# Performance work log

Hardware: AMD Instinct MI355X
Metric: run time of the kernel (lower is better)

The kernel has to match this reference:

```python
import jax, jax.numpy as jnp
import numpy as np

N_HEADS = 8
D_MODEL = 256
HEAD_DEPTH = D_MODEL // N_HEADS
B, S = 2, 4096


def setup_inputs() -> dict:
    key = jax.random.key(0)
    ks = jax.random.split(key, 8)
    scale = 1.0 / np.sqrt(D_MODEL)
    return {
        "q": jax.random.normal(ks[0], (B, S, D_MODEL), dtype=jnp.float32),
        "k": jax.random.normal(ks[1], (B, S, D_MODEL), dtype=jnp.float32),
        "v": jax.random.normal(ks[2], (B, S, D_MODEL), dtype=jnp.float32),
        "mask": jax.random.randint(ks[3], (B, S, S), 0, 2).astype(jnp.bool_),
        "wq": jax.random.normal(ks[4], (D_MODEL, D_MODEL), dtype=jnp.float32) * scale,
        "wk": jax.random.normal(ks[5], (D_MODEL, D_MODEL), dtype=jnp.float32) * scale,
        "wv": jax.random.normal(ks[6], (D_MODEL, D_MODEL), dtype=jnp.float32) * scale,
        "w_out": jax.random.normal(ks[7], (D_MODEL, D_MODEL), dtype=jnp.float32) * scale,
    }


def _split_heads(x):
    # [B, S, D] -> [B, H, S, Dh]
    b, s, _ = x.shape
    return x.reshape(b, s, N_HEADS, HEAD_DEPTH).transpose(0, 2, 1, 3)


def reference(q, k, v, mask, wq, wk, wv, w_out):
    Q = _split_heads(q @ wq)
    K = _split_heads(k @ wk)
    V = _split_heads(v @ wv)
    # [B, H, Sq, Sk]
    scores = jnp.einsum('bhqd,bhkd->bhqk', Q, K) / jnp.sqrt(
        jnp.asarray(HEAD_DEPTH, dtype=Q.dtype))
    # mask True -> -inf, broadcast over heads
    scores = jnp.where(mask[:, None, :, :], -jnp.inf, scores)
    probs = jax.nn.softmax(scores, axis=-1)
    attn = jnp.einsum('bhqk,bhkd->bhqd', probs, V)
    attn = attn.transpose(0, 2, 1, 3).reshape(q.shape[0], -1, D_MODEL)
    return attn @ w_out
```

## Files before the change

kernel.cpp:

```cpp
#include <hip/hip_runtime.h>
#include <stdint.h>

typedef __bf16 bf16;
typedef __bf16 bf16x8 __attribute__((ext_vector_type(8)));
typedef __bf16 bf16x4 __attribute__((ext_vector_type(4)));
typedef float  f32x4  __attribute__((ext_vector_type(4)));
typedef float  f32x8  __attribute__((ext_vector_type(8)));
typedef float  f32x16 __attribute__((ext_vector_type(16)));
typedef float  float4v __attribute__((ext_vector_type(4)));
typedef int    int4v   __attribute__((ext_vector_type(4)));
typedef unsigned int uint;
typedef unsigned long long ull;

#define QSCALE 0.25505003984214403f


__global__ __launch_bounds__(256) void transpose_w(
    const float* __restrict__ w0, const float* __restrict__ w1,
    const float* __restrict__ w2, const float* __restrict__ w3,
    bf16* __restrict__ WT) {
  const int wsel = blockIdx.z;
  const float* W = wsel == 0 ? w0 : wsel == 1 ? w1 : wsel == 2 ? w2 : w3;
  const int k0 = blockIdx.x * 64, n0 = blockIdx.y * 64;
  __shared__ __align__(16) bf16 t[64][72];
  const int tid = threadIdx.x;
  {
    const int kk = (tid >> 4) << 2;
    const int nn = (tid & 15) << 2;
#pragma unroll
    for (int r = 0; r < 4; ++r) {
      float4v a = *(const float4v*)(W + (size_t)(k0 + kk + r) * 256 + n0 + nn);
#pragma unroll
      for (int j = 0; j < 4; ++j) t[nn + j][kk + r] = (bf16)a[j];
    }
  }
  __syncthreads();
  {
    const int ni = tid >> 2;
    const int c  = (tid & 3) * 16;
    bf16x8 o0 = *(const bf16x8*)(&t[ni][c]);
    bf16x8 o1 = *(const bf16x8*)(&t[ni][c + 8]);
    bf16* dst = WT + (size_t)wsel * 65536 + (size_t)(n0 + ni) * 256 + k0 + c;
    *(bf16x8*)dst = o0;
    *(bf16x8*)(dst + 8) = o1;
  }
}

__global__ __launch_bounds__(256) void proj_pack(
    const float* __restrict__ xq, const float* __restrict__ xk, const float* __restrict__ xv,
    const bf16* __restrict__ WT,
    bf16* __restrict__ Qp, bf16* __restrict__ Kp, bf16* __restrict__ Vp,
    const int* __restrict__ mask, uint* __restrict__ M2) {
  __shared__ __align__(16) unsigned char smem[18432];
  const int tid = threadIdx.x;

  if (blockIdx.x >= 768) {
    uint* lds32 = (uint*)smem;
    const int pid = blockIdx.x - 768;
    const int bb = pid >> 8;
    const int qt = (pid >> 2) & 63, kc = pid & 3;
    const int q0 = qt * 64;
    const int w = tid >> 6, l = tid & 63;
#pragma unroll 2
    for (int r = 0; r < 16; ++r) {
      const int row = w * 16 + r;
      const size_t rowbase = ((size_t)(bb * 4096 + q0 + row)) * 4096 + kc * 1024;
      uint u = 0;
#pragma unroll
      for (int i = 0; i < 4; ++i) {
        int4v m = *(const int4v*)(mask + rowbase + i * 256 + l * 4);
        uint nib = (m[0] != 0 ? 1u : 0u) | (m[1] != 0 ? 2u : 0u) |
                   (m[2] != 0 ? 4u : 0u) | (m[3] != 0 ? 8u : 0u);
        u |= nib << (i * 8);
      }
      lds32[row * 65 + l] = u;
    }
    __syncthreads();
    {
      const int q = tid & 63, kg = tid >> 6;
      const uint* lrow = lds32 + q * 65;
      const int sh = kg * 8;
      uint* o = M2 + ((size_t)(bb * 128 + kc * 32 + kg * 8)) * 4096 + q0 + q;
#pragma unroll
      for (int j = 0; j < 8; ++j) {
        uint d = 0;
#pragma unroll
        for (int jj = 0; jj < 8; ++jj) {
          const uint wv = lrow[j * 8 + jj];
          d |= ((wv >> sh) & 0xFu) << (jj * 4);
        }
        o[(size_t)j * 4096] = d;
      }
    }
    return;
  }

  const int z = blockIdx.x >> 8;
  const int r8 = blockIdx.x & 255;
  const int m0 = (r8 >> 1) * 64, n0 = (r8 & 1) * 128;
  const float* X = z == 0 ? xq : (z == 1 ? xk : xv);
  const bf16* wt = WT + (size_t)z * 65536;
  const int wave = tid >> 6, lane = tid & 63;
  const int nl = lane & 15, quad = lane >> 4;
  const int arow = m0 + wave * 16 + nl;
  const float* xrow = X + (size_t)arow * 256;

  f32x4 zero4 = {0.f, 0.f, 0.f, 0.f};
  f32x4 acc[8];
#pragma unroll
  for (int i = 0; i < 8; ++i) acc[i] = zero4;

  for (int ks = 0; ks < 8; ++ks) {
    float4v a0 = *(const float4v*)(xrow + ks * 32 + quad * 8);
    float4v a1 = *(const float4v*)(xrow + ks * 32 + quad * 8 + 4);
    bf16x8 af;
#pragma unroll
    for (int i = 0; i < 4; ++i) { af[i] = (bf16)a0[i]; af[4 + i] = (bf16)a1[i]; }
#pragma unroll
    for (int nf = 0; nf < 8; ++nf) {
      bf16x8 bfr = *(const bf16x8*)(wt + (size_t)(n0 + nf * 16 + nl) * 256 + ks * 32 + quad * 8);
      acc[nf] = __builtin_amdgcn_mfma_f32_16x16x32_bf16(af, bfr, acc[nf], 0, 0, 0);
    }
  }

  const int bq = m0 >> 12;
  const int s0 = m0 & 4095;
  const int posl = wave * 16 + quad * 4;

  if (z == 2) {
    bf16* tv = (bf16*)smem;
#pragma unroll
    for (int nf = 0; nf < 8; ++nf) {
      const int col = nf * 16 + nl;
      bf16x4 o;
#pragma unroll
      for (int rr = 0; rr < 4; ++rr) o[rr] = (bf16)acc[nf][rr];
      *(bf16x4*)(tv + (size_t)col * 72 + posl) = o;
    }
    __syncthreads();
    const int h2 = tid >> 6, ln = tid & 63;
    const int d = ln & 31, shalf = ln >> 5;
    const int h = (n0 >> 5) + h2;
    bf16* vb = Vp + (size_t)(bq * 8 + h) * 131072 + (size_t)(s0 >> 5) * 1024 + d * 8;
#pragma unroll
    for (int it = 0; it < 4; ++it) {
      const int blk = it >> 1, sub = (it & 1) * 2 + shalf;
      const int K0 = (sub >> 1) * 16 + (sub & 1) * 4;
      const bf16* src = tv + (size_t)(h2 * 32 + d) * 72 + blk * 32 + K0;
      bf16x4 g0 = *(const bf16x4*)(src);
      bf16x4 g1 = *(const bf16x4*)(src + 8);
      bf16x8 o;
#pragma unroll
      for (int j = 0; j < 4; ++j) { o[j] = g0[j]; o[4 + j] = g1[j]; }
      *(bf16x8*)(vb + (size_t)blk * 1024 + sub * 256) = o;
    }
  } else {
    bf16* tq = (bf16*)smem;
    const float scale = (z == 0) ? QSCALE : 1.0f;
#pragma unroll
    for (int nf = 0; nf < 8; ++nf) {
      const int col = nf * 16 + nl;
#pragma unroll
      for (int rr = 0; rr < 4; ++rr)
        tq[(size_t)(posl + rr) * 136 + col] = (bf16)(acc[nf][rr] * scale);
    }
    __syncthreads();
    bf16* Out = z == 0 ? Qp : Kp;
    const int h2 = tid >> 6, ln = tid & 63;
    const int h = (n0 >> 5) + h2;
    const int s = s0 + ln;
    bf16* ob = Out + (size_t)(bq * 8 + h) * 131072 + (size_t)(s >> 5) * 1024 + (s & 31) * 8;
#pragma unroll
    for (int sub = 0; sub < 4; ++sub) {
      bf16x8 o = *(const bf16x8*)(tq + (size_t)ln * 136 + h2 * 32 + sub * 8);
      *(bf16x8*)(ob + sub * 256) = o;
    }
  }
}

__global__ __launch_bounds__(256, 4) void attn_kernel(
    const bf16* __restrict__ Qp, const bf16* __restrict__ Kp,
    const bf16* __restrict__ Vp, const uint* __restrict__ M2,
    bf16* __restrict__ Og) {
  const int id = blockIdx.x;
  const int xcd = id & 7, slot = id >> 3;
  const int bh = xcd * 2 + (slot >> 6);
  const int q0 = (slot & 63) * 64;
  const int b = bh >> 3, h = bh & 7;
  const int tid = threadIdx.x, w = tid >> 6, lane = tid & 63;
  const int nl = lane & 31, half = lane >> 5;
  const int qsub = w & 1, kh = w >> 1;

  __shared__ float Ored[4][32][33];
  __shared__ float Lsum[32][4];

  const size_t bhbase = (size_t)bh * 131072;
  const int so0 = half * 256 + nl * 8;
  const int so1 = 512 + half * 256 + nl * 8;

  bf16x8 qf0, qf1;
  {
    const bf16* qb = Qp + bhbase + (size_t)((q0 >> 5) + qsub) * 1024;
    qf0 = *(const bf16x8*)(qb + so0);
    qf1 = *(const bf16x8*)(qb + so1);
  }

  const bf16* Kw = Kp + bhbase + (size_t)kh * 65536;
  const bf16* Vw = Vp + bhbase + (size_t)kh * 65536;
  const uint* Mw = M2 + (size_t)b * 524288 + (size_t)kh * 262144 + q0 + qsub * 32 + nl;

  f32x16 acc, lacc;
#pragma unroll
  for (int i = 0; i < 16; ++i) { acc[i] = 0.f; lacc[i] = 0.f; }

  bf16x8 ones;
#pragma unroll
  for (int i = 0; i < 8; ++i) ones[i] = (bf16)1.0f;

  struct Frag { bf16x8 ka0, ka1, va0, va1; uint m0; };
  auto LOADF = [&](int kt) -> Frag {
    Frag f;
    const bf16* kc = Kw + (size_t)kt * 1024;
    const bf16* vc = Vw + (size_t)kt * 1024;
    f.ka0 = *(const bf16x8*)(kc + so0);
    f.ka1 = *(const bf16x8*)(kc + so1);
    f.va0 = *(const bf16x8*)(vc + so0);
    f.va1 = *(const bf16x8*)(vc + so1);
    f.m0 = Mw[(size_t)kt * 4096];
    return f;
  };

  auto STEP = [&](const Frag& f) {
    const int mpos = (int)(f.m0 >> (4 * half));
    f32x16 bias;
#pragma unroll
    for (int g = 0; g < 4; ++g)
#pragma unroll
      for (int r = 0; r < 4; ++r) {
        const int i = g * 4 + r, off = r + 8 * g;
        const uint mb = (uint)__builtin_amdgcn_sbfe(mpos, off, 1);
        bias[i] = __uint_as_float(mb & 0xFF800000u);
      }
    __builtin_amdgcn_s_setprio(1);
    f32x16 st = __builtin_amdgcn_mfma_f32_32x32x16_bf16(f.ka0, qf0, bias, 0, 0, 0);
    st = __builtin_amdgcn_mfma_f32_32x32x16_bf16(f.ka1, qf1, st, 0, 0, 0);
    __builtin_amdgcn_s_setprio(0);

    f32x16 pf;
#pragma unroll
    for (int i = 0; i < 16; ++i) pf[i] = __builtin_amdgcn_exp2f(st[i]);

    const bf16x8 pb0 = __builtin_convertvector(
        __builtin_shufflevector(pf, pf, 0, 1, 2, 3, 4, 5, 6, 7), bf16x8);
    const bf16x8 pb1 = __builtin_convertvector(
        __builtin_shufflevector(pf, pf, 8, 9, 10, 11, 12, 13, 14, 15), bf16x8);

    __builtin_amdgcn_s_setprio(1);
    acc  = __builtin_amdgcn_mfma_f32_32x32x16_bf16(f.va0, pb0, acc, 0, 0, 0);
    acc  = __builtin_amdgcn_mfma_f32_32x32x16_bf16(f.va1, pb1, acc, 0, 0, 0);
    lacc = __builtin_amdgcn_mfma_f32_32x32x16_bf16(ones, pb0, lacc, 0, 0, 0);
    lacc = __builtin_amdgcn_mfma_f32_32x32x16_bf16(ones, pb1, lacc, 0, 0, 0);
    __builtin_amdgcn_s_setprio(0);
  };

  Frag fa = LOADF(0), fb;
  for (int kt = 0; kt < 64; kt += 2) {
    if (kt && !(kt & 3)) __builtin_amdgcn_s_barrier();
    fb = LOADF(kt + 1);
    STEP(fa);
    if (kt + 2 < 64) fa = LOADF(kt + 2);
    STEP(fb);
  }

#pragma unroll
  for (int g = 0; g < 4; ++g)
#pragma unroll
    for (int r = 0; r < 4; ++r) {
      const int d = r + 8 * g + 4 * half, i = g * 4 + r;
      Ored[w][d][nl] = acc[i];
    }
  if (half == 0) Lsum[nl][w] = lacc[0];
  __syncthreads();
  {
    const int q = tid >> 2, d0 = (tid & 3) * 8;
    const int qq = q & 31, qs = q >> 5;
    const float s = Lsum[qq][qs] + Lsum[qq][qs + 2];
    const float rl = 1.0f / s;
    bf16x8 o;
#pragma unroll
    for (int dj = 0; dj < 8; ++dj) {
      const int d = d0 + dj;
      const float sum = Ored[qs][d][qq] + Ored[qs + 2][d][qq];
      o[dj] = (bf16)(sum * rl);
    }
    *(bf16x8*)(Og + ((size_t)(b * 4096 + q0 + q)) * 256 + h * 32 + d0) = o;
  }
}

__global__ __launch_bounds__(256) void gemm_out(
    const bf16* __restrict__ A, const bf16* __restrict__ WTo, float* __restrict__ C) {
  const int m0 = blockIdx.x * 64, n0 = blockIdx.y * 64;
  const int tid = threadIdx.x, wave = tid >> 6, lane = tid & 63;
  const int nl = lane & 15, quad = lane >> 4;
  const int arow = m0 + wave * 16 + nl;

  f32x4 zero4 = {0.f, 0.f, 0.f, 0.f};
  f32x4 acc[4];
#pragma unroll
  for (int i = 0; i < 4; ++i) acc[i] = zero4;

  for (int ks = 0; ks < 8; ++ks) {
    bf16x8 af = *(const bf16x8*)(A + (size_t)arow * 256 + ks * 32 + quad * 8);
#pragma unroll
    for (int nf = 0; nf < 4; ++nf) {
      bf16x8 bfr = *(const bf16x8*)(WTo + (size_t)(n0 + nf * 16 + nl) * 256 + ks * 32 + quad * 8);
      acc[nf] = __builtin_amdgcn_mfma_f32_16x16x32_bf16(af, bfr, acc[nf], 0, 0, 0);
    }
  }
  const int Rbase = m0 + wave * 16 + quad * 4;
#pragma unroll
  for (int nf = 0; nf < 4; ++nf)
#pragma unroll
    for (int r = 0; r < 4; ++r)
      C[(size_t)(Rbase + r) * 256 + n0 + nf * 16 + nl] = acc[nf][r];
}

extern "C" void kernel_launch(void* const* d_in, const int* in_sizes, int n_in,
                              void* d_out, int out_size, void* d_ws, size_t ws_size,
                              hipStream_t stream) {
  const float* q  = (const float*)d_in[0];
  const float* k  = (const float*)d_in[1];
  const float* v  = (const float*)d_in[2];
  const int*  mask = (const int*)d_in[3];
  const float* wq = (const float*)d_in[4];
  const float* wk = (const float*)d_in[5];
  const float* wv = (const float*)d_in[6];
  const float* wo = (const float*)d_in[7];
  float* out = (float*)d_out;

  uint8_t* ws = (uint8_t*)d_ws;
  bf16* WT = (bf16*)ws;
  bf16* Qp = (bf16*)(ws + (512u << 10));
  bf16* Kp = Qp + 2097152;
  bf16* Vp = Kp + 2097152;
  uint* Mb = (uint*)((uint8_t*)(Vp + 2097152));
  bf16* Ao = (bf16*)((uint8_t*)Mb + (4u << 20));

  transpose_w<<<dim3(4, 4, 4), 256, 0, stream>>>(wq, wk, wv, wo, WT);
  proj_pack<<<dim3(768 + 512), 256, 0, stream>>>(q, k, v, WT, Qp, Kp, Vp, mask, Mb);
  attn_kernel<<<dim3(1024), 256, 0, stream>>>(Qp, Kp, Vp, Mb, Ao);
  gemm_out<<<dim3(128, 4), 256, 0, stream>>>(Ao, WT + 3 * 65536, out);
}
```

Before: 310.8 us.

## Replace MFMA row-sum with VALU sums, deepen prefetch, reorder mask-pack blocks

The attention kernel stops computing the softmax denominator with two extra MFMAs against a ones vector. It accumulates the exp values in registers per lane and reduces them through a widened shared-memory Lsum array. The K/V/mask prefetch becomes a 4-deep rotating register pipeline without the periodic s_barrier. The mask-packing blocks are moved ahead of the projection blocks so the long mask stream starts first, and launch bounds and unroll counts are tweaked. Deeper prefetch raises register pressure, which could hurt occupancy at 4 blocks per CU.

```diff
diff --git a/kernel.cpp b/kernel.cpp
--- a/kernel.cpp
+++ b/kernel.cpp
@@ -46,7 +46,7 @@
   }
 }
 
-__global__ __launch_bounds__(256) void proj_pack(
+__global__ __launch_bounds__(256, 2) void proj_pack(
     const float* __restrict__ xq, const float* __restrict__ xk, const float* __restrict__ xv,
     const bf16* __restrict__ WT,
     bf16* __restrict__ Qp, bf16* __restrict__ Kp, bf16* __restrict__ Vp,
@@ -54,14 +54,14 @@
   __shared__ __align__(16) unsigned char smem[18432];
   const int tid = threadIdx.x;
 
-  if (blockIdx.x >= 768) {
+  if (blockIdx.x < 512) {
     uint* lds32 = (uint*)smem;
-    const int pid = blockIdx.x - 768;
+    const int pid = blockIdx.x;
     const int bb = pid >> 8;
     const int qt = (pid >> 2) & 63, kc = pid & 3;
     const int q0 = qt * 64;
     const int w = tid >> 6, l = tid & 63;
-#pragma unroll 2
+#pragma unroll 8
     for (int r = 0; r < 16; ++r) {
       const int row = w * 16 + r;
       const size_t rowbase = ((size_t)(bb * 4096 + q0 + row)) * 4096 + kc * 1024;
@@ -95,8 +95,9 @@
     return;
   }
 
-  const int z = blockIdx.x >> 8;
-  const int r8 = blockIdx.x & 255;
+  const int pid2 = blockIdx.x - 512;
+  const int z = pid2 >> 8;
+  const int r8 = pid2 & 255;
   const int m0 = (r8 >> 1) * 64, n0 = (r8 & 1) * 128;
   const float* X = z == 0 ? xq : (z == 1 ? xk : xv);
   const bf16* wt = WT + (size_t)z * 65536;
@@ -192,7 +193,7 @@
   const int qsub = w & 1, kh = w >> 1;
 
   __shared__ float Ored[4][32][33];
-  __shared__ float Lsum[32][4];
+  __shared__ float Lsum[32][8];
 
   const size_t bhbase = (size_t)bh * 131072;
   const int so0 = half * 256 + nl * 8;
@@ -209,13 +210,10 @@
   const bf16* Vw = Vp + bhbase + (size_t)kh * 65536;
   const uint* Mw = M2 + (size_t)b * 524288 + (size_t)kh * 262144 + q0 + qsub * 32 + nl;
 
-  f32x16 acc, lacc;
-#pragma unroll
-  for (int i = 0; i < 16; ++i) { acc[i] = 0.f; lacc[i] = 0.f; }
-
-  bf16x8 ones;
-#pragma unroll
-  for (int i = 0; i < 8; ++i) ones[i] = (bf16)1.0f;
+  f32x16 acc;
+#pragma unroll
+  for (int i = 0; i < 16; ++i) acc[i] = 0.f;
+  f32x4 ls = {0.f, 0.f, 0.f, 0.f};
 
   struct Frag { bf16x8 ka0, ka1, va0, va1; uint m0; };
   auto LOADF = [&](int kt) -> Frag {
@@ -248,7 +246,14 @@
 
     f32x16 pf;
 #pragma unroll
-    for (int i = 0; i < 16; ++i) pf[i] = __builtin_amdgcn_exp2f(st[i]);
+    for (int g = 0; g < 4; ++g)
+#pragma unroll
+      for (int r = 0; r < 4; ++r) {
+        const int i = g * 4 + r;
+        const float e = __builtin_amdgcn_exp2f(st[i]);
+        ls[g] += e;
+        pf[i] = e;
+      }
 
     const bf16x8 pb0 = __builtin_convertvector(
         __builtin_shufflevector(pf, pf, 0, 1, 2, 3, 4, 5, 6, 7), bf16x8);
@@ -256,20 +261,17 @@
         __builtin_shufflevector(pf, pf, 8, 9, 10, 11, 12, 13, 14, 15), bf16x8);
 
     __builtin_amdgcn_s_setprio(1);
-    acc  = __builtin_amdgcn_mfma_f32_32x32x16_bf16(f.va0, pb0, acc, 0, 0, 0);
-    acc  = __builtin_amdgcn_mfma_f32_32x32x16_bf16(f.va1, pb1, acc, 0, 0, 0);
-    lacc = __builtin_amdgcn_mfma_f32_32x32x16_bf16(ones, pb0, lacc, 0, 0, 0);
-    lacc = __builtin_amdgcn_mfma_f32_32x32x16_bf16(ones, pb1, lacc, 0, 0, 0);
+    acc = __builtin_amdgcn_mfma_f32_32x32x16_bf16(f.va0, pb0, acc, 0, 0, 0);
+    acc = __builtin_amdgcn_mfma_f32_32x32x16_bf16(f.va1, pb1, acc, 0, 0, 0);
     __builtin_amdgcn_s_setprio(0);
   };
 
-  Frag fa = LOADF(0), fb;
-  for (int kt = 0; kt < 64; kt += 2) {
-    if (kt && !(kt & 3)) __builtin_amdgcn_s_barrier();
-    fb = LOADF(kt + 1);
-    STEP(fa);
-    if (kt + 2 < 64) fa = LOADF(kt + 2);
-    STEP(fb);
+  Frag f0 = LOADF(0), f1 = LOADF(1), f2 = LOADF(2), f3 = LOADF(3);
+  for (int kt = 0; kt < 64; kt += 4) {
+    STEP(f0); if (kt + 4 < 64) f0 = LOADF(kt + 4);
+    STEP(f1); if (kt + 5 < 64) f1 = LOADF(kt + 5);
+    STEP(f2); if (kt + 6 < 64) f2 = LOADF(kt + 6);
+    STEP(f3); if (kt + 7 < 64) f3 = LOADF(kt + 7);
   }
 
 #pragma unroll
@@ -279,12 +281,13 @@
       const int d = r + 8 * g + 4 * half, i = g * 4 + r;
       Ored[w][d][nl] = acc[i];
     }
-  if (half == 0) Lsum[nl][w] = lacc[0];
+  Lsum[nl][w * 2 + half] = (ls[0] + ls[1]) + (ls[2] + ls[3]);
   __syncthreads();
   {
     const int q = tid >> 2, d0 = (tid & 3) * 8;
     const int qq = q & 31, qs = q >> 5;
-    const float s = Lsum[qq][qs] + Lsum[qq][qs + 2];
+    const float s = (Lsum[qq][qs * 2] + Lsum[qq][qs * 2 + 1]) +
+                    (Lsum[qq][(qs + 2) * 2] + Lsum[qq][(qs + 2) * 2 + 1]);
     const float rl = 1.0f / s;
     bf16x8 o;
 #pragma unroll
@@ -297,7 +300,7 @@
   }
 }
 
-__global__ __launch_bounds__(256) void gemm_out(
+__global__ __launch_bounds__(256, 2) void gemm_out(
     const bf16* __restrict__ A, const bf16* __restrict__ WTo, float* __restrict__ C) {
   const int m0 = blockIdx.x * 64, n0 = blockIdx.y * 64;
   const int tid = threadIdx.x, wave = tid >> 6, lane = tid & 63;
@@ -347,7 +350,7 @@
   bf16* Ao = (bf16*)((uint8_t*)Mb + (4u << 20));
 
   transpose_w<<<dim3(4, 4, 4), 256, 0, stream>>>(wq, wk, wv, wo, WT);
-  proj_pack<<<dim3(768 + 512), 256, 0, stream>>>(q, k, v, WT, Qp, Kp, Vp, mask, Mb);
+  proj_pack<<<dim3(512 + 768), 256, 0, stream>>>(q, k, v, WT, Qp, Kp, Vp, mask, Mb);
   attn_kernel<<<dim3(1024), 256, 0, stream>>>(Qp, Kp, Vp, Mb, Ao);
   gemm_out<<<dim3(128, 4), 256, 0, stream>>>(Ao, WT + 3 * 65536, out);
 }
```

After: 541.8 us. 1.74x slower.
